# Optimization experiments

Measured on AMD Instinct MI355X. Metric: run time of the kernel, lower is better.

## Reference

```python
import jax, jax.numpy as jnp
import numpy as np

# AdEx constants (from source module)
T_REF = 2e-3
CM = 281e-12
GL = 30e-9
EL = -70.6e-3
VT = -50.4e-3
DELTAT = 2e-3
TAUW = 144e-3
A = 4e-9
B = 0.0805e-9
DT = 1e-3
REF_STEPS = int(round(T_REF / DT))  # 2 steps


def setup_inputs() -> dict:
    key = jax.random.key(0)
    T, N = 500, 100000
    # input current ~ nanoamps so a fraction of neurons spike
    I = jax.random.normal(key, (T, N), dtype=jnp.float32) * 0.5e-9 + 0.5e-9
    v0 = jnp.full((N,), EL, dtype=jnp.float32)      # membrane potential at rest
    c0 = jnp.zeros((N,), dtype=jnp.float32)         # adaptation variable
    ref0 = jnp.zeros((N,), dtype=jnp.int32)         # refractory counters
    return {"I": I, "v0": v0, "c0": c0, "ref0": ref0}


def reference(I, v0, c0, ref0):
    """AdEx neuron simulation: scan over T timesteps, [N] state vectors.
    Returns v_trace of shape [T, N]."""

    def step(carry, I_t):
        v, c, ref = carry
        in_ref = ref > 0
        # refractory neurons are clamped to EL (tf.where(ref_op, EL, v))
        v_eff = jnp.where(in_ref, EL, v)
        # AdEx membrane dynamics (forward Euler); exp arg clipped for safety
        exp_term = GL * DELTAT * jnp.exp(jnp.minimum((v_eff - VT) / DELTAT, 15.0))
        dv = (DT / CM) * (-GL * (v_eff - EL) + exp_term - c + I_t)
        v_new = jnp.where(in_ref, EL, v_eff + dv)
        # adaptation current dynamics
        c_new = c + (DT / TAUW) * (A * (v_eff - EL) - c)
        # spike detection + reset
        spike = v_new >= VT
        v_out = jnp.where(spike, EL, v_new)
        c_out = jnp.where(spike, c_new + B, c_new)
        ref_new = jnp.where(spike, REF_STEPS, jnp.maximum(ref - 1, 0))
        return (v_out, c_out, ref_new), v_out

    (_, _, _), v_trace = jax.lax.scan(step, (v0, c0, ref0), I)
    return v_trace
```

## Files before the change

### kernel.cpp

```cpp
#include <hip/hip_runtime.h>


#define DEPTH 10

__global__ __launch_bounds__(256) void adex_kernel(
    const float* __restrict__ I,
    const float* __restrict__ v0,
    const float* __restrict__ c0,
    const int*   __restrict__ ref0,
    float*       __restrict__ out,
    int N, int T)
{
#pragma clang fp contract(off)
    const float EL      = (float)(-70.6e-3);
    const float VT      = (float)(-50.4e-3);
    const float DELTAT  = (float)(2e-3);
    const float NEG_GL  = (float)(-30e-9);
    const float GLDT    = (float)(30e-9 * 2e-3);
    const float DT_CM   = (float)(1e-3 / 281e-12);
    const float DT_TAUW = (float)(1e-3 / 144e-3);
    const float Af      = (float)(4e-9);
    const float Bf      = (float)(0.0805e-9);
    const int   REF_STEPS = 2;

    int n = blockIdx.x * blockDim.x + threadIdx.x;
    if (n >= N) return;

    float v  = v0[n];
    float c  = c0[n];
    int   rf = ref0[n];

    size_t stride    = (size_t)N;
    size_t load_idx  = (size_t)n;
    size_t store_idx = (size_t)n;

    auto step = [&](float It) -> float {
        bool  in_ref = rf > 0;
        float v_eff  = in_ref ? EL : v;

        float arg      = fminf((v_eff - VT) / DELTAT, 15.0f);
        float exp_term = GLDT * __expf(arg) ;
        exp_term = GLDT * expf(arg);

        float acc = NEG_GL * (v_eff - EL);
        acc = acc + exp_term;
        acc = acc - c;
        acc = acc + It;
        float dv = DT_CM * acc;

        float v_new = in_ref ? EL : (v_eff + dv);
        float c_new = c + DT_TAUW * ((Af * (v_eff - EL)) - c);

        bool  spike = v_new >= VT;
        float v_out = spike ? EL : v_new;

        c  = spike ? (c_new + Bf) : c_new;
        rf = spike ? REF_STEPS : (in_ref ? rf - 1 : 0);
        v  = v_out;
        return v_out;
    };

    float buf[DEPTH];

#pragma unroll
    for (int k = 0; k < DEPTH; ++k) {
        if (k < T) { buf[k] = I[load_idx]; load_idx += stride; }
    }

    int t = 0;
    for (; t + 2 * DEPTH <= T; t += DEPTH) {
#pragma unroll
        for (int j = 0; j < DEPTH; ++j) {
            float It = buf[j];
            buf[j] = I[load_idx]; load_idx += stride;
            float v_out = step(It);
            __builtin_nontemporal_store(v_out, &out[store_idx]);
            store_idx += stride;
        }
    }

#pragma unroll
    for (int j = 0; j < 2 * DEPTH; ++j) {
        if (t + j < T) {
            float It = buf[j % DEPTH];
            if (t + j + DEPTH < T) { buf[j % DEPTH] = I[load_idx]; load_idx += stride; }
            float v_out = step(It);
            __builtin_nontemporal_store(v_out, &out[store_idx]);
            store_idx += stride;
        }
    }
}

extern "C" void kernel_launch(void* const* d_in, const int* in_sizes, int n_in,
                              void* d_out, int out_size, void* d_ws, size_t ws_size,
                              hipStream_t stream) {
    const float* I    = (const float*)d_in[0];
    const float* v0   = (const float*)d_in[1];
    const float* c0   = (const float*)d_in[2];
    const int*   ref0 = (const int*)d_in[3];
    float*       out  = (float*)d_out;

    int N = in_sizes[1];
    int T = in_sizes[0] / N;

    dim3 block(256);
    dim3 grid((N + 255) / 256);
    adex_kernel<<<grid, block, 0, stream>>>(I, v0, c0, ref0, out, N, T);
}
```

Baseline: 351.8 us.

## Shrink blocks, deepen prefetch, use 32-bit offsets and reciprocal-based division

```diff
diff --git a/kernel.cpp b/kernel.cpp
--- a/kernel.cpp
+++ b/kernel.cpp
@@ -1,9 +1,9 @@
 #include <hip/hip_runtime.h>
 
 
-#define DEPTH 10
+#define DEPTH 12
 
-__global__ __launch_bounds__(256) void adex_kernel(
+__global__ __launch_bounds__(64) void adex_kernel(
     const float* __restrict__ I,
     const float* __restrict__ v0,
     const float* __restrict__ c0,
@@ -12,15 +12,16 @@
     int N, int T)
 {
 #pragma clang fp contract(off)
-    const float EL      = (float)(-70.6e-3);
-    const float VT      = (float)(-50.4e-3);
-    const float DELTAT  = (float)(2e-3);
-    const float NEG_GL  = (float)(-30e-9);
-    const float GLDT    = (float)(30e-9 * 2e-3);
-    const float DT_CM   = (float)(1e-3 / 281e-12);
-    const float DT_TAUW = (float)(1e-3 / 144e-3);
-    const float Af      = (float)(4e-9);
-    const float Bf      = (float)(0.0805e-9);
+    const float EL       = (float)(-70.6e-3);
+    const float VT       = (float)(-50.4e-3);
+    const float DELTAT   = (float)(2e-3);
+    const float R_DELTAT = (float)(1.0 / (double)((float)(2e-3)));
+    const float NEG_GL   = (float)(-30e-9);
+    const float GLDT     = (float)(30e-9 * 2e-3);
+    const float DT_CM    = (float)(1e-3 / 281e-12);
+    const float DT_TAUW  = (float)(1e-3 / 144e-3);
+    const float Af       = (float)(4e-9);
+    const float Bf       = (float)(0.0805e-9);
     const int   REF_STEPS = 2;
 
     int n = blockIdx.x * blockDim.x + threadIdx.x;
@@ -30,17 +31,27 @@
     float c  = c0[n];
     int   rf = ref0[n];
 
-    size_t stride    = (size_t)N;
-    size_t load_idx  = (size_t)n;
-    size_t store_idx = (size_t)n;
+    const unsigned stride_b = (unsigned)N * 4u;
+    unsigned load_off  = (unsigned)n * 4u;
+    unsigned store_off = load_off;
+
+    auto ld = [&](unsigned off) -> float {
+        return *(const float*)((const char*)I + off);
+    };
+    auto st = [&](unsigned off, float val) {
+        __builtin_nontemporal_store(val, (float*)((char*)out + off));
+    };
 
     auto step = [&](float It) -> float {
         bool  in_ref = rf > 0;
         float v_eff  = in_ref ? EL : v;
 
-        float arg      = fminf((v_eff - VT) / DELTAT, 15.0f);
-        float exp_term = GLDT * __expf(arg) ;
-        exp_term = GLDT * expf(arg);
+        float x   = v_eff - VT;
+        float y0  = x * R_DELTAT;
+        float e   = fmaf(-DELTAT, y0, x);
+        float arg = fmaf(e, R_DELTAT, y0);
+        arg = fminf(arg, 15.0f);
+        float exp_term = GLDT * expf(arg);
 
         float acc = NEG_GL * (v_eff - EL);
         acc = acc + exp_term;
@@ -64,7 +75,7 @@
 
 #pragma unroll
     for (int k = 0; k < DEPTH; ++k) {
-        if (k < T) { buf[k] = I[load_idx]; load_idx += stride; }
+        if (k < T) { buf[k] = ld(load_off); load_off += stride_b; }
     }
 
     int t = 0;
@@ -72,10 +83,10 @@
 #pragma unroll
         for (int j = 0; j < DEPTH; ++j) {
             float It = buf[j];
-            buf[j] = I[load_idx]; load_idx += stride;
+            buf[j] = ld(load_off); load_off += stride_b;
             float v_out = step(It);
-            __builtin_nontemporal_store(v_out, &out[store_idx]);
-            store_idx += stride;
+            st(store_off, v_out);
+            store_off += stride_b;
         }
     }
 
@@ -83,10 +94,10 @@
     for (int j = 0; j < 2 * DEPTH; ++j) {
         if (t + j < T) {
             float It = buf[j % DEPTH];
-            if (t + j + DEPTH < T) { buf[j % DEPTH] = I[load_idx]; load_idx += stride; }
+            if (t + j + DEPTH < T) { buf[j % DEPTH] = ld(load_off); load_off += stride_b; }
             float v_out = step(It);
-            __builtin_nontemporal_store(v_out, &out[store_idx]);
-            store_idx += stride;
+            st(store_off, v_out);
+            store_off += stride_b;
         }
     }
 }
@@ -103,7 +114,7 @@
     int N = in_sizes[1];
     int T = in_sizes[0] / N;
 
-    dim3 block(256);
-    dim3 grid((N + 255) / 256);
+    dim3 block(64);
+    dim3 grid((N + 63) / 64);
     adex_kernel<<<grid, block, 0, stream>>>(I, v0, c0, ref0, out, N, T);
 }
```

Result: no change. 347.2 us (-1.3%).
